# Kernel optimization log

Measured on AMD Instinct MI355X. Metric: run time of the kernel, lower is better.

The kernel has to match this reference:

```python
import jax, jax.numpy as jnp
import numpy as np

N_NODES = 50000
N_EDGES = 1600000
D_IN = 128
D_OUT = 128
EPS = 0.001  # GINConv(eps=0.001) hard-coded in the module


def setup_inputs() -> dict:
    key = jax.random.key(0)
    k_x, k_e, k_w1, k_b1, k_w2, k_b2 = jax.random.split(key, 6)
    x = jax.random.normal(k_x, (N_NODES, D_IN), dtype=jnp.float32)
    edge_index = jax.random.randint(k_e, (2, N_EDGES), 0, N_NODES, dtype=jnp.int64)
    # MLP params (nn.Linear default init scale ~ 1/sqrt(fan_in))
    s1 = 1.0 / np.sqrt(D_IN)
    s2 = 1.0 / np.sqrt(D_OUT)
    W1 = jax.random.uniform(k_w1, (D_IN, D_OUT), jnp.float32, -s1, s1)
    b1 = jax.random.uniform(k_b1, (D_OUT,), jnp.float32, -s1, s1)
    W2 = jax.random.uniform(k_w2, (D_OUT, D_OUT), jnp.float32, -s2, s2)
    b2 = jax.random.uniform(k_b2, (D_OUT,), jnp.float32, -s2, s2)
    return {"x": x, "edge_index": edge_index, "W1": W1, "b1": b1, "W2": W2, "b2": b2}


def reference(x, edge_index, W1, b1, W2, b2):
    # GIN: out = MLP((1 + eps) * x + sum_{j in N(i)} x_j)
    src = edge_index[0]  # message source nodes
    dst = edge_index[1]  # aggregation targets
    agg = jax.ops.segment_sum(x[src], dst, num_segments=x.shape[0])  # [N, D_IN]
    h = (1.0 + EPS) * x + agg
    h = jax.nn.relu(h @ W1 + b1)
    return h @ W2 + b2
```

## Files before the change

kernel.cpp:

```cpp
#include <hip/hip_runtime.h>
#include <hip/hip_bf16.h>


#define N_NODES 50000
#define N_EDGES 1600000
#define D 128

#define SB 196
#define SCH 8192
#define BSH 6
#define BSZ 64
#define KB 782
#define CAPB 2560
#define HP 136

typedef __attribute__((ext_vector_type(8))) short short8;
typedef __attribute__((ext_vector_type(4))) float float4v;

__device__ inline unsigned short f2b(float f) {
    unsigned u = __builtin_bit_cast(unsigned, f);
    u = u + 0x7fffu + ((u >> 16) & 1u);
    return (unsigned short)(u >> 16);
}
__device__ inline float b2f_lo(unsigned u) { return __builtin_bit_cast(float, u << 16); }
__device__ inline float b2f_hi(unsigned u) { return __builtin_bit_cast(float, u & 0xffff0000u); }

#define LPAD 136

__global__ __launch_bounds__(1024) void k_prep(const float* __restrict__ W1,
                                               const float* __restrict__ W2,
                                               unsigned short* __restrict__ Wt1,
                                               unsigned short* __restrict__ Wt2,
                                               unsigned* __restrict__ bpos,
                                               const int* __restrict__ ei,
                                               int* __restrict__ flag) {
    int bb = blockIdx.x;
    if (bb == 0) {
        __shared__ int nz;
        if (threadIdx.x == 0) nz = 0;
        __syncthreads();
        if (threadIdx.x < 256 && ei[threadIdx.x * 2 + 1] != 0) atomicAdd(&nz, 1);
        __syncthreads();
        if (threadIdx.x == 0) *flag = (nz == 0) ? 1 : 0;
        for (int i = threadIdx.x; i < KB; i += 1024) bpos[i] = 0u;
    }
    const float* W = (bb < 4) ? W1 : W2;
    unsigned short* Wt = (bb < 4) ? Wt1 : Wt2;
    int q = bb & 3;
    for (int i = q * 4096 + threadIdx.x; i < (q + 1) * 4096; i += 1024) {
        int k = i >> 7;
        int n = i & 127;
        Wt[n * 128 + k] = f2b(W[k * 128 + n]);
    }
}

__global__ __launch_bounds__(256, 2) void k_mm(const float* __restrict__ Av,
                                               const unsigned short* __restrict__ Wtg,
                                               unsigned short* __restrict__ y, int M) {
    __shared__ short Al[128 * LPAD];
    __shared__ short Wt[128 * LPAD];

    int t = threadIdx.x;
    int row0 = blockIdx.x * 128;

    const float4* X4 = (const float4*)Av;
    #pragma unroll
    for (int i = 0; i < 16; ++i) {
        int idx = i * 256 + t;
        int r = idx >> 5;
        int c = idx & 31;
        float4 v = make_float4(0.f, 0.f, 0.f, 0.f);
        if (row0 + r < M) v = X4[(size_t)(row0 + r) * 32 + c];
        short4 o;
        o.x = (short)f2b(v.x); o.y = (short)f2b(v.y);
        o.z = (short)f2b(v.z); o.w = (short)f2b(v.w);
        *(short4*)&Al[r * LPAD + c * 4] = o;
    }
    {
        const uint4* Wg4 = (const uint4*)Wtg;
        #pragma unroll
        for (int i = 0; i < 8; ++i) {
            int idx = i * 256 + t;
            int r = idx >> 4;
            int c = idx & 15;
            *(uint4*)&Wt[r * LPAD + c * 8] = Wg4[idx];
        }
    }
    __syncthreads();

    int wave = t >> 6;
    int lane = t & 63;
    int quad = lane >> 4;
    int l16 = lane & 15;
    int rowbase = wave * 32;

    float4v acc[2][8];
    #pragma unroll
    for (int mt = 0; mt < 2; ++mt)
        #pragma unroll
        for (int nt = 0; nt < 8; ++nt)
            acc[mt][nt] = (float4v){0.f, 0.f, 0.f, 0.f};

    #pragma unroll
    for (int kc = 0; kc < 4; ++kc) {
        int koff = kc * 32 + quad * 8;
        short8 a0 = *(const short8*)&Al[(rowbase + l16) * LPAD + koff];
        short8 a1 = *(const short8*)&Al[(rowbase + 16 + l16) * LPAD + koff];
        #pragma unroll
        for (int nt = 0; nt < 8; ++nt) {
            short8 bfr = *(const short8*)&Wt[(nt * 16 + l16) * LPAD + koff];
            acc[0][nt] = __builtin_amdgcn_mfma_f32_16x16x32_bf16(a0, bfr, acc[0][nt], 0, 0, 0);
            acc[1][nt] = __builtin_amdgcn_mfma_f32_16x16x32_bf16(a1, bfr, acc[1][nt], 0, 0, 0);
        }
    }

    #pragma unroll
    for (int mt = 0; mt < 2; ++mt) {
        int rloc = rowbase + mt * 16 + quad * 4;
        #pragma unroll
        for (int nt = 0; nt < 8; ++nt) {
            int col = nt * 16 + l16;
            #pragma unroll
            for (int r = 0; r < 4; ++r) {
                int grow = row0 + rloc + r;
                if (grow < M)
                    y[(size_t)grow * 128 + col] = f2b(acc[mt][nt][r]);
            }
        }
    }
}

__global__ __launch_bounds__(1024) void k_sort(const int* __restrict__ ei,
                                               const int* __restrict__ flag,
                                               unsigned* __restrict__ bpos,
                                               unsigned* __restrict__ pairs) {
    __shared__ unsigned hist[KB];
    int b = blockIdx.x;
    int t = threadIdx.x;
    for (int i = t; i < KB; i += 1024) hist[i] = 0u;
    __syncthreads();
    int wide = *flag;
    int e0 = b * SCH + t * 8;
    int dv[8], sv[8], rv[8];
    if (e0 < N_EDGES) {
        if (wide) {
            const uint4* pd = (const uint4*)&ei[((size_t)N_EDGES + e0) * 2];
            const uint4* ps = (const uint4*)&ei[(size_t)e0 * 2];
            #pragma unroll
            for (int j = 0; j < 4; ++j) {
                uint4 qd = pd[j], qs = ps[j];
                dv[2 * j] = (int)qd.x; dv[2 * j + 1] = (int)qd.z;
                sv[2 * j] = (int)qs.x; sv[2 * j + 1] = (int)qs.z;
            }
        } else {
            const uint4* pd = (const uint4*)&ei[(size_t)N_EDGES + e0];
            const uint4* ps = (const uint4*)&ei[e0];
            #pragma unroll
            for (int j = 0; j < 2; ++j) {
                uint4 qd = pd[j], qs = ps[j];
                dv[4 * j] = (int)qd.x; dv[4 * j + 1] = (int)qd.y;
                dv[4 * j + 2] = (int)qd.z; dv[4 * j + 3] = (int)qd.w;
                sv[4 * j] = (int)qs.x; sv[4 * j + 1] = (int)qs.y;
                sv[4 * j + 2] = (int)qs.z; sv[4 * j + 3] = (int)qs.w;
            }
        }
    } else {
        #pragma unroll
        for (int i = 0; i < 8; ++i) dv[i] = -1;
    }
    #pragma unroll
    for (int i = 0; i < 8; ++i) {
        if ((unsigned)dv[i] < (unsigned)N_NODES) {
            rv[i] = (int)atomicAdd(&hist[dv[i] >> BSH], 1u);
            if ((unsigned)sv[i] >= (unsigned)N_NODES) sv[i] = 0;
        } else dv[i] = -1;
    }
    __syncthreads();
    for (int i = t; i < KB; i += 1024) {
        unsigned c = hist[i];
        hist[i] = c ? atomicAdd(&bpos[i], c) : 0u;
    }
    __syncthreads();
    #pragma unroll
    for (int i = 0; i < 8; ++i) {
        if (dv[i] >= 0) {
            int kb = dv[i] >> BSH;
            unsigned r = hist[kb] + (unsigned)rv[i];
            if (r < CAPB)
                pairs[(size_t)kb * CAPB + r] =
                    (unsigned)sv[i] | ((unsigned)(dv[i] & (BSZ - 1)) << 17);
        }
    }
}

__global__ __launch_bounds__(512) void k_bgather(const unsigned short* __restrict__ y,
                                                 const unsigned* __restrict__ pairs,
                                                 const unsigned* __restrict__ bpos,
                                                 const float* __restrict__ b1,
                                                 const unsigned short* __restrict__ Wt2g,
                                                 const float* __restrict__ b2,
                                                 float* __restrict__ out) {
    __shared__ unsigned sbuf[CAPB];
    __shared__ short htile[BSZ * HP];
    __shared__ int cnt[BSZ], loff[BSZ], pos[BSZ];
    int k = blockIdx.x;
    int t = threadIdx.x;
    if (t < BSZ) cnt[t] = 0;
    __syncthreads();
    int beg = k * CAPB;
    int tot = (int)bpos[k];
    if (tot > CAPB) tot = CAPB;
    for (int i = t; i < tot; i += 512)
        atomicAdd(&cnt[pairs[beg + i] >> 17], 1);
    __syncthreads();
    if (t < BSZ) {
        int v = cnt[t];
        int xs = v;
        #pragma unroll
        for (int off = 1; off < 64; off <<= 1) {
            int u0 = __shfl_up(xs, off, 64);
            if (t >= off) xs += u0;
        }
        loff[t] = xs - v;
        pos[t] = xs - v;
    }
    __syncthreads();
    for (int i = t; i < tot; i += 512) {
        unsigned p = pairs[beg + i];
        int r = atomicAdd(&pos[p >> 17], 1);
        sbuf[r] = p & 0x1FFFFu;
    }
    __syncthreads();

    int w = t >> 6;
    int lane = t & 63;
    int g = lane >> 5;
    int u = lane & 31;
    const uint2* yr = (const uint2*)y;

    #pragma unroll 1
    for (int q = 0; q < 8; ++q) {
        int dl = w * 8 + q;
        int node = (k << BSH) + dl;
        int jb = loff[dl];
        int je = jb + cnt[dl];
        float a0 = 0.f, a1 = 0.f, a2 = 0.f, a3 = 0.f;
        int j = jb + g;
        for (; j + 14 < je; j += 16) {
            int ss[8];
            #pragma unroll
            for (int q2 = 0; q2 < 8; ++q2) ss[q2] = (int)sbuf[j + 2 * q2];
            #pragma unroll
            for (int q2 = 0; q2 < 8; ++q2) {
                uint2 A = yr[(size_t)ss[q2] * 32 + u];
                a0 += b2f_lo(A.x); a1 += b2f_hi(A.x);
                a2 += b2f_lo(A.y); a3 += b2f_hi(A.y);
            }
        }
        for (; j < je; j += 2) {
            uint2 A = yr[(size_t)sbuf[j] * 32 + u];
            a0 += b2f_lo(A.x); a1 += b2f_hi(A.x);
            a2 += b2f_lo(A.y); a3 += b2f_hi(A.y);
        }
        a0 += __shfl_xor(a0, 32, 64); a1 += __shfl_xor(a1, 32, 64);
        a2 += __shfl_xor(a2, 32, 64); a3 += __shfl_xor(a3, 32, 64);
        if (g == 0) {
            uint2 o = make_uint2(0u, 0u);
            if (node < N_NODES) {
                uint2 S = yr[(size_t)node * 32 + u];
                float4 bv = ((const float4*)b1)[u];
                float f0 = fmaf(1.001f, b2f_lo(S.x), a0) + bv.x;
                float f1 = fmaf(1.001f, b2f_hi(S.x), a1) + bv.y;
                float f2 = fmaf(1.001f, b2f_lo(S.y), a2) + bv.z;
                float f3 = fmaf(1.001f, b2f_hi(S.y), a3) + bv.w;
                f0 = fmaxf(f0, 0.f); f1 = fmaxf(f1, 0.f);
                f2 = fmaxf(f2, 0.f); f3 = fmaxf(f3, 0.f);
                o.x = (unsigned)f2b(f0) | ((unsigned)f2b(f1) << 16);
                o.y = (unsigned)f2b(f2) | ((unsigned)f2b(f3) << 16);
            }
            *(uint2*)&htile[dl * HP + u * 4] = o;
        }
    }
    __syncthreads();

    int quad = lane >> 4;
    int l16 = lane & 15;
    int mt = w >> 1;
    int nh = w & 1;
    float4v accB[4];
    #pragma unroll
    for (int nt2 = 0; nt2 < 4; ++nt2) accB[nt2] = (float4v){0.f, 0.f, 0.f, 0.f};
    #pragma unroll
    for (int kc = 0; kc < 4; ++kc) {
        int koff = kc * 32 + quad * 8;
        short8 a = *(const short8*)&htile[(mt * 16 + l16) * HP + koff];
        #pragma unroll
        for (int nt2 = 0; nt2 < 4; ++nt2) {
            int col = nh * 64 + nt2 * 16 + l16;
            short8 bfr = *(const short8*)&Wt2g[col * 128 + koff];
            accB[nt2] = __builtin_amdgcn_mfma_f32_16x16x32_bf16(a, bfr, accB[nt2], 0, 0, 0);
        }
    }
    int node0 = k << BSH;
    #pragma unroll
    for (int nt2 = 0; nt2 < 4; ++nt2) {
        int col = nh * 64 + nt2 * 16 + l16;
        float bb = b2[col];
        #pragma unroll
        for (int r = 0; r < 4; ++r) {
            int grow = node0 + mt * 16 + quad * 4 + r;
            if (grow < N_NODES)
                out[(size_t)grow * 128 + col] = accB[nt2][r] + bb;
        }
    }
}

extern "C" void kernel_launch(void* const* d_in, const int* in_sizes, int n_in,
                              void* d_out, int out_size, void* d_ws, size_t ws_size,
                              hipStream_t stream) {
    const float* x  = (const float*)d_in[0];
    const int*   ei = (const int*)d_in[1];
    const float* W1 = (const float*)d_in[2];
    const float* b1 = (const float*)d_in[3];
    const float* W2 = (const float*)d_in[4];
    const float* b2 = (const float*)d_in[5];
    float* out = (float*)d_out;

    char* ws = (char*)d_ws;
    unsigned short* y       = (unsigned short*)(ws);
    unsigned*       pairs   = (unsigned*)(ws + 12800000);
    unsigned*       bpos    = (unsigned*)(ws + 21000000);
    unsigned short* Wt1     = (unsigned short*)(ws + 21100000);
    unsigned short* Wt2     = (unsigned short*)(ws + 21200000);
    int*            flag    = (int*)    (ws + 21300000);

    int gblocks = (N_NODES + 127) / 128;

    k_prep<<<8, 1024, 0, stream>>>(W1, W2, Wt1, Wt2, bpos, ei, flag);
    k_mm<<<gblocks, 256, 0, stream>>>(x, Wt1, y, N_NODES);
    k_sort<<<SB, 1024, 0, stream>>>(ei, flag, bpos, pairs);
    k_bgather<<<KB, 512, 0, stream>>>(y, pairs, bpos, b1, Wt2, b2, out);
}
```

Before: 194.2 us.

## Fuse first GEMM and edge bucketing into one heterogeneous kernel launch

Merges the x@W1 GEMM kernel and the edge bucket-sort kernel into one launch. The first blocks run the GEMM and the remaining blocks sort edges, so the two independent stages can overlap on the GPU and one launch gap disappears. The GEMM also drops its LDS staging: each wave loads its x rows directly into registers, converts them to bf16, and reads W1 fragments straight from global memory. Sort blocks shrink to 512 threads with half-size edge chunks. The risks are redundant global reads of W1 and less reuse per block.

```diff
diff --git a/kernel.cpp b/kernel.cpp
--- a/kernel.cpp
+++ b/kernel.cpp
@@ -6,8 +6,9 @@
 #define N_EDGES 1600000
 #define D 128
 
-#define SB 196
-#define SCH 8192
+#define MMB 391
+#define SCH 4096
+#define NSB 391
 #define BSH 6
 #define BSZ 64
 #define KB 782
@@ -24,8 +25,6 @@
 }
 __device__ inline float b2f_lo(unsigned u) { return __builtin_bit_cast(float, u << 16); }
 __device__ inline float b2f_hi(unsigned u) { return __builtin_bit_cast(float, u & 0xffff0000u); }
-
-#define LPAD 136
 
 __global__ __launch_bounds__(1024) void k_prep(const float* __restrict__ W1,
                                                const float* __restrict__ W2,
@@ -54,90 +53,65 @@
     }
 }
 
-__global__ __launch_bounds__(256, 2) void k_mm(const float* __restrict__ Av,
-                                               const unsigned short* __restrict__ Wtg,
-                                               unsigned short* __restrict__ y, int M) {
-    __shared__ short Al[128 * LPAD];
-    __shared__ short Wt[128 * LPAD];
-
+__global__ __launch_bounds__(512) void k_mmsort(const float* __restrict__ x,
+                                                const unsigned short* __restrict__ Wt1g,
+                                                unsigned short* __restrict__ y,
+                                                const int* __restrict__ ei,
+                                                const int* __restrict__ flag,
+                                                unsigned* __restrict__ bpos,
+                                                unsigned* __restrict__ pairs) {
+    __shared__ unsigned hist[KB];
+    int bid = blockIdx.x;
     int t = threadIdx.x;
-    int row0 = blockIdx.x * 128;
-
-    const float4* X4 = (const float4*)Av;
-    #pragma unroll
-    for (int i = 0; i < 16; ++i) {
-        int idx = i * 256 + t;
-        int r = idx >> 5;
-        int c = idx & 31;
-        float4 v = make_float4(0.f, 0.f, 0.f, 0.f);
-        if (row0 + r < M) v = X4[(size_t)(row0 + r) * 32 + c];
-        short4 o;
-        o.x = (short)f2b(v.x); o.y = (short)f2b(v.y);
-        o.z = (short)f2b(v.z); o.w = (short)f2b(v.w);
-        *(short4*)&Al[r * LPAD + c * 4] = o;
-    }
-    {
-        const uint4* Wg4 = (const uint4*)Wtg;
-        #pragma unroll
-        for (int i = 0; i < 8; ++i) {
-            int idx = i * 256 + t;
-            int r = idx >> 4;
-            int c = idx & 15;
-            *(uint4*)&Wt[r * LPAD + c * 8] = Wg4[idx];
-        }
-    }
-    __syncthreads();
-
-    int wave = t >> 6;
-    int lane = t & 63;
-    int quad = lane >> 4;
-    int l16 = lane & 15;
-    int rowbase = wave * 32;
-
-    float4v acc[2][8];
-    #pragma unroll
-    for (int mt = 0; mt < 2; ++mt)
-        #pragma unroll
-        for (int nt = 0; nt < 8; ++nt)
-            acc[mt][nt] = (float4v){0.f, 0.f, 0.f, 0.f};
-
-    #pragma unroll
-    for (int kc = 0; kc < 4; ++kc) {
-        int koff = kc * 32 + quad * 8;
-        short8 a0 = *(const short8*)&Al[(rowbase + l16) * LPAD + koff];
-        short8 a1 = *(const short8*)&Al[(rowbase + 16 + l16) * LPAD + koff];
-        #pragma unroll
-        for (int nt = 0; nt < 8; ++nt) {
-            short8 bfr = *(const short8*)&Wt[(nt * 16 + l16) * LPAD + koff];
-            acc[0][nt] = __builtin_amdgcn_mfma_f32_16x16x32_bf16(a0, bfr, acc[0][nt], 0, 0, 0);
-            acc[1][nt] = __builtin_amdgcn_mfma_f32_16x16x32_bf16(a1, bfr, acc[1][nt], 0, 0, 0);
-        }
-    }
-
-    #pragma unroll
-    for (int mt = 0; mt < 2; ++mt) {
-        int rloc = rowbase + mt * 16 + quad * 4;
+
+    if (bid < MMB) {
+        int row0 = bid * 128;
+        int w = t >> 6;
+        int lane = t & 63;
+        int quad = lane >> 4;
+        int l16 = lane & 15;
+        int arow = row0 + w * 16 + l16;
+        const float* xrow = x + (size_t)arow * 128;
+
+        float4v acc[8];
+        #pragma unroll
+        for (int nt = 0; nt < 8; ++nt) acc[nt] = (float4v){0.f, 0.f, 0.f, 0.f};
+
+        #pragma unroll
+        for (int kc = 0; kc < 4; ++kc) {
+            int koff = kc * 32 + quad * 8;
+            float4 v0 = make_float4(0.f, 0.f, 0.f, 0.f);
+            float4 v1 = make_float4(0.f, 0.f, 0.f, 0.f);
+            if (arow < N_NODES) {
+                v0 = *(const float4*)&xrow[koff];
+                v1 = *(const float4*)&xrow[koff + 4];
+            }
+            short8 a;
+            a[0] = (short)f2b(v0.x); a[1] = (short)f2b(v0.y);
+            a[2] = (short)f2b(v0.z); a[3] = (short)f2b(v0.w);
+            a[4] = (short)f2b(v1.x); a[5] = (short)f2b(v1.y);
+            a[6] = (short)f2b(v1.z); a[7] = (short)f2b(v1.w);
+            #pragma unroll
+            for (int nt = 0; nt < 8; ++nt) {
+                short8 bfr = *(const short8*)&Wt1g[(nt * 16 + l16) * 128 + koff];
+                acc[nt] = __builtin_amdgcn_mfma_f32_16x16x32_bf16(a, bfr, acc[nt], 0, 0, 0);
+            }
+        }
         #pragma unroll
         for (int nt = 0; nt < 8; ++nt) {
             int col = nt * 16 + l16;
             #pragma unroll
             for (int r = 0; r < 4; ++r) {
-                int grow = row0 + rloc + r;
-                if (grow < M)
-                    y[(size_t)grow * 128 + col] = f2b(acc[mt][nt][r]);
-            }
-        }
-    }
-}
-
-__global__ __launch_bounds__(1024) void k_sort(const int* __restrict__ ei,
-                                               const int* __restrict__ flag,
-                                               unsigned* __restrict__ bpos,
-                                               unsigned* __restrict__ pairs) {
-    __shared__ unsigned hist[KB];
-    int b = blockIdx.x;
-    int t = threadIdx.x;
-    for (int i = t; i < KB; i += 1024) hist[i] = 0u;
+                int grow = row0 + w * 16 + quad * 4 + r;
+                if (grow < N_NODES)
+                    y[(size_t)grow * 128 + col] = f2b(acc[nt][r]);
+            }
+        }
+        return;
+    }
+
+    int b = bid - MMB;
+    for (int i = t; i < KB; i += 512) hist[i] = 0u;
     __syncthreads();
     int wide = *flag;
     int e0 = b * SCH + t * 8;
@@ -176,7 +150,7 @@
         } else dv[i] = -1;
     }
     __syncthreads();
-    for (int i = t; i < KB; i += 1024) {
+    for (int i = t; i < KB; i += 512) {
         unsigned c = hist[i];
         hist[i] = c ? atomicAdd(&bpos[i], c) : 0u;
     }
@@ -334,10 +308,7 @@
     unsigned short* Wt2     = (unsigned short*)(ws + 21200000);
     int*            flag    = (int*)    (ws + 21300000);
 
-    int gblocks = (N_NODES + 127) / 128;
-
     k_prep<<<8, 1024, 0, stream>>>(W1, W2, Wt1, Wt2, bpos, ei, flag);
-    k_mm<<<gblocks, 256, 0, stream>>>(x, Wt1, y, N_NODES);
-    k_sort<<<SB, 1024, 0, stream>>>(ei, flag, bpos, pairs);
+    k_mmsort<<<MMB + NSB, 512, 0, stream>>>(x, Wt1, y, ei, flag, bpos, pairs);
     k_bgather<<<KB, 512, 0, stream>>>(y, pairs, bpos, b1, Wt2, b2, out);
 }
```

Result: slower. 199.4 us (+2.7%).
